# Kernel optimization log

Hardware: AMD Instinct MI355X
Metric: run time of the kernel (lower is better)

## Reference

```python
import jax, jax.numpy as jnp
import numpy as np

N = 50000      # nodes
E = 800000     # edges
D_IN = 128     # in_channels == hidden_channels
D_H = 128
R = 4          # num_relations
L = 3          # n_layers
D_MID = D_H // 4
D_OUT = 40
BN_EPS = 1e-5


def setup_inputs() -> dict:
    key = jax.random.key(0)
    ks = jax.random.split(key, 12)
    return {
        "x": jax.random.normal(ks[0], (N, D_IN), dtype=jnp.float32),
        "edge_index": jax.random.randint(ks[1], (2, E), 0, N, dtype=jnp.int64),
        "edge_type": jax.random.randint(ks[2], (E,), 0, R, dtype=jnp.int64),
        "W_skip": jax.random.normal(ks[3], (L, D_IN, D_H), dtype=jnp.float32) * 0.1,
        "W_film_skip": jax.random.normal(ks[4], (L, D_IN, 2 * D_H), dtype=jnp.float32) * 0.1,
        "W_rel": jax.random.normal(ks[5], (L, R, D_IN, D_H), dtype=jnp.float32) * 0.1,
        "W_film": jax.random.normal(ks[6], (L, R, D_IN, 2 * D_H), dtype=jnp.float32) * 0.1,
        "bn_w": jnp.ones((L, D_H), dtype=jnp.float32),
        "bn_b": jnp.zeros((L, D_H), dtype=jnp.float32),
        "lin1_w": jax.random.normal(ks[7], (D_H, D_MID), dtype=jnp.float32) * 0.1,
        "lin1_b": jnp.zeros((D_MID,), dtype=jnp.float32),
        "lin2_w": jax.random.normal(ks[8], (D_MID, D_OUT), dtype=jnp.float32) * 0.1,
        "lin2_b": jnp.zeros((D_OUT,), dtype=jnp.float32),
    }


def _film_conv(x, Wsk, Wfsk, Wr, Wf, src, dst, etype):
    # Self path: FiLM-modulated skip transform (PyG FiLMConv, act=ReLU).
    beta_s, gamma_s = jnp.split(x @ Wfsk, 2, axis=-1)  # split order: beta, gamma
    out = jax.nn.relu(gamma_s * (x @ Wsk) + beta_s)    # [N, D_H]
    # Per-relation node transforms (small GEMMs, avoids dynamic edge masking).
    xr = jnp.einsum('ni,rio->nro', x, Wr)              # [N, R, D_H]
    bg = jnp.einsum('ni,rio->nro', x, Wf)              # [N, R, 2*D_H]
    beta, gamma = jnp.split(bg, 2, axis=-1)            # each [N, R, D_H]
    # Messages: gamma_i * (W_r x_j) + beta_i, relation chosen per edge.
    msg = jax.nn.relu(gamma[dst, etype] * xr[src, etype] + beta[dst, etype])  # [E, D_H]
    # Mean aggregation per (target node, relation) subgraph, then sum relations.
    seg = dst * R + etype
    sums = jax.ops.segment_sum(msg, seg, num_segments=N * R)
    cnts = jax.ops.segment_sum(jnp.ones((msg.shape[0],), msg.dtype), seg, num_segments=N * R)
    mean = sums / jnp.maximum(cnts, 1.0)[:, None]      # [N*R, D_H]
    return out + mean.reshape(N, R, D_H).sum(axis=1)


def _batchnorm(h, w, b):
    mu = h.mean(axis=0)
    var = ((h - mu) ** 2).mean(axis=0)  # biased variance, as torch BN training
    return (h - mu) * jax.lax.rsqrt(var + BN_EPS) * w + b


def reference(x, edge_index, edge_type, W_skip, W_film_skip, W_rel, W_film,
              bn_w, bn_b, lin1_w, lin1_b, lin2_w, lin2_b):
    src, dst = edge_index[0], edge_index[1]
    h = x
    for l in range(L):
        h = _film_conv(h, W_skip[l], W_film_skip[l], W_rel[l], W_film[l], src, dst, edge_type)
        h = _batchnorm(h, bn_w[l], bn_b[l])
        # dropout treated as identity (deterministic reference)
    h = jax.nn.leaky_relu(h @ lin1_w + lin1_b, negative_slope=0.2)
    return h @ lin2_w + lin2_b
```

## Files before the change

### kernel.cpp

```cpp
#include <hip/hip_runtime.h>

#define N_NODES 50000
#define N_EDGES 800000
#define D 128
#define R_REL 4
#define L_LAYERS 3
#define M_SEG (N_NODES * R_REL)
#define NCOLS 384
#define BN_EPS 1e-5f

typedef unsigned short u16;
typedef __attribute__((ext_vector_type(8))) short short8v;
typedef __attribute__((ext_vector_type(4))) float f32x4;

static __device__ __forceinline__ u16 f2b(float f) {
    union { float f; unsigned int u; } a; a.f = f;
    unsigned int u = a.u;
    return (u16)((u + 0x7FFFu + ((u >> 16) & 1u)) >> 16);
}
static __device__ __forceinline__ float b2f(u16 b) {
    union { unsigned int u; float f; } a; a.u = ((unsigned int)b) << 16;
    return a.f;
}

__global__ void pack_w(const float* __restrict__ Wsk, const float* __restrict__ Wfsk,
                       const float* __restrict__ Wr, const float* __restrict__ Wf,
                       u16* __restrict__ Wpb) {
    int idx = blockIdx.x * 256 + threadIdx.x;
    if (idx >= L_LAYERS * 5 * NCOLS * D) return;
    int k = idx & 127;
    int rem = idx >> 7;
    int j = rem % NCOLS;
    int lp = rem / NCOLS;
    int l = lp / 5, p = lp % 5;
    float v;
    if (p == 0) {
        v = (j < D) ? Wsk[(l * D + k) * D + j] : Wfsk[(l * D + k) * 2 * D + (j - D)];
    } else {
        int r = p - 1;
        v = (j < D) ? Wr[((l * R_REL + r) * D + k) * D + j]
                    : Wf[((l * R_REL + r) * D + k) * 2 * D + (j - D)];
    }
    Wpb[idx] = f2b(v);
}

__global__ void cvt_bf16(const float* __restrict__ x, u16* __restrict__ xb) {
    int idx = blockIdx.x * 256 + threadIdx.x;
    if (idx >= N_NODES * D) return;
    xb[idx] = f2b(x[idx]);
}

__global__ void hist_k(const int* __restrict__ dst, const int* __restrict__ et,
                       int* __restrict__ cnt, int* __restrict__ rank) {
    int e = blockIdx.x * 256 + threadIdx.x;
    if (e >= N_EDGES) return;
    rank[e] = atomicAdd(&cnt[dst[e] * R_REL + et[e]], 1);
}

__global__ void scan_a(const int* __restrict__ cnt, int* __restrict__ bsum) {
    __shared__ int sm[256];
    int t = threadIdx.x;
    int idx = blockIdx.x * 256 + t;
    sm[t] = (idx < M_SEG) ? cnt[idx] : 0;
    __syncthreads();
    for (int s = 128; s > 0; s >>= 1) {
        if (t < s) sm[t] += sm[t + s];
        __syncthreads();
    }
    if (t == 0) bsum[blockIdx.x] = sm[0];
}

#define NB_SCAN 782
__global__ void scan_b(const int* __restrict__ bsum, int* __restrict__ bsumex, int* __restrict__ offs) {
    __shared__ int sm[1024];
    int t = threadIdx.x;
    int v = (t < NB_SCAN) ? bsum[t] : 0;
    sm[t] = v;
    __syncthreads();
    for (int d = 1; d < 1024; d <<= 1) {
        int add = (t >= d) ? sm[t - d] : 0;
        __syncthreads();
        sm[t] += add;
        __syncthreads();
    }
    if (t < NB_SCAN) bsumex[t] = sm[t] - v;
    if (t == NB_SCAN - 1) offs[M_SEG] = sm[t];
}

__global__ void scan_c(const int* __restrict__ cnt, const int* __restrict__ bsumex, int* __restrict__ offs) {
    __shared__ int sm[256];
    int t = threadIdx.x;
    int idx = blockIdx.x * 256 + t;
    int v = (idx < M_SEG) ? cnt[idx] : 0;
    sm[t] = v;
    __syncthreads();
    for (int d = 1; d < 256; d <<= 1) {
        int add = (t >= d) ? sm[t - d] : 0;
        __syncthreads();
        sm[t] += add;
        __syncthreads();
    }
    if (idx < M_SEG) offs[idx] = bsumex[blockIdx.x] + sm[t] - v;
}

__global__ void scatter_k(const int* __restrict__ src, const int* __restrict__ dst,
                          const int* __restrict__ et, const int* __restrict__ offs,
                          const int* __restrict__ rank, int* __restrict__ esrc) {
    int e = blockIdx.x * 256 + threadIdx.x;
    if (e >= N_EDGES) return;
    int seg = dst[e] * R_REL + et[e];
    esrc[offs[seg] + rank[e]] = src[e];
}

__global__ __launch_bounds__(512) void gemm_planes(const uint4* __restrict__ Aq,
                                                   const uint4* __restrict__ Bq,
                                                   u16* __restrict__ bufR) {
    __shared__ uint4 As[128 * 16];
    __shared__ u16 Cs[128 * 128];
    int t = threadIdx.x;
    int m0 = blockIdx.x * 128;
    int p = blockIdx.y;
#pragma unroll
    for (int i = 0; i < 4; ++i) {
        int idx = i * 512 + t;
        int row = idx >> 4, kk = idx & 15;
        int gr = m0 + row;
        if (gr >= N_NODES) gr = N_NODES - 1;
        As[(row << 4) + (kk ^ (row & 7))] = Aq[gr * 16 + kk];
    }
    __syncthreads();
    int lane = t & 63, w = t >> 6;
    int wr = w >> 2, wc = w & 3;
    int lr = lane & 15, lh = lane >> 4;
    short8v a[4][4];
#pragma unroll
    for (int m = 0; m < 4; ++m) {
        int row = wr * 64 + m * 16 + lr;
#pragma unroll
        for (int ks = 0; ks < 4; ++ks)
            a[m][ks] = *reinterpret_cast<const short8v*>(&As[(row << 4) + ((ks * 4 + lh) ^ (row & 7))]);
    }
    const uint4* Bp = Bq + (size_t)(1 + p) * NCOLS * 16;
    u16* Cp = bufR + (size_t)p * N_NODES * NCOLS;
    f32x4 zero = {0.f, 0.f, 0.f, 0.f};
    int srow = t >> 4, sslot = t & 15;
#pragma unroll
    for (int chunk = 0; chunk < 3; ++chunk) {
        int n0 = chunk * 128;
        f32x4 acc[4][2];
#pragma unroll
        for (int m = 0; m < 4; ++m)
#pragma unroll
            for (int n = 0; n < 2; ++n) acc[m][n] = zero;
#pragma unroll
        for (int ks = 0; ks < 4; ++ks) {
            short8v b[2];
#pragma unroll
            for (int n = 0; n < 2; ++n) {
                int row = n0 + wc * 32 + n * 16 + lr;
                b[n] = *reinterpret_cast<const short8v*>(&Bp[row * 16 + ks * 4 + lh]);
            }
#pragma unroll
            for (int m = 0; m < 4; ++m)
#pragma unroll
                for (int n = 0; n < 2; ++n)
                    acc[m][n] = __builtin_amdgcn_mfma_f32_16x16x32_bf16(a[m][ks], b[n], acc[m][n], 0, 0, 0);
        }
        __syncthreads();
#pragma unroll
        for (int m = 0; m < 4; ++m)
#pragma unroll
            for (int reg = 0; reg < 4; ++reg) {
                int row = wr * 64 + m * 16 + lh * 4 + reg;
#pragma unroll
                for (int n = 0; n < 2; ++n) {
                    int col = wc * 32 + n * 16 + lr;
                    Cs[row * 128 + (col ^ ((lh & 1) << 4))] = f2b(acc[m][n][reg]);
                }
            }
        __syncthreads();
#pragma unroll
        for (int it = 0; it < 4; ++it) {
            int row = it * 32 + srow;
            int gr = m0 + row;
            if (gr < N_NODES) {
                uint4 v = *reinterpret_cast<const uint4*>(
                    &Cs[row * 128 + ((sslot * 8) ^ (((row >> 2) & 1) << 4))]);
                *reinterpret_cast<uint4*>(&Cp[(size_t)gr * NCOLS + n0 + sslot * 8]) = v;
            }
        }
    }
}

__global__ __launch_bounds__(512) void gemm_self(const uint4* __restrict__ Aq,
                                                 const uint4* __restrict__ Bq,
                                                 u16* __restrict__ selfb) {
    __shared__ uint4 As[128 * 16];
    __shared__ u16 Cs[128 * 128];
    int t = threadIdx.x;
    int m0 = blockIdx.x * 128;
#pragma unroll
    for (int i = 0; i < 4; ++i) {
        int idx = i * 512 + t;
        int row = idx >> 4, kk = idx & 15;
        int gr = m0 + row;
        if (gr >= N_NODES) gr = N_NODES - 1;
        As[(row << 4) + (kk ^ (row & 7))] = Aq[gr * 16 + kk];
    }
    __syncthreads();
    int lane = t & 63, w = t >> 6;
    int wr = w >> 2, wc = w & 3;
    int lr = lane & 15, lh = lane >> 4;
    short8v a[4][4];
#pragma unroll
    for (int m = 0; m < 4; ++m) {
        int row = wr * 64 + m * 16 + lr;
#pragma unroll
        for (int ks = 0; ks < 4; ++ks)
            a[m][ks] = *reinterpret_cast<const short8v*>(&As[(row << 4) + ((ks * 4 + lh) ^ (row & 7))]);
    }
    f32x4 zero = {0.f, 0.f, 0.f, 0.f};
    f32x4 hx[4][2], hb[4][2];
#pragma unroll
    for (int chunk = 0; chunk < 3; ++chunk) {
        int n0 = chunk * 128;
        f32x4 acc[4][2];
#pragma unroll
        for (int m = 0; m < 4; ++m)
#pragma unroll
            for (int n = 0; n < 2; ++n) acc[m][n] = zero;
#pragma unroll
        for (int ks = 0; ks < 4; ++ks) {
            short8v b[2];
#pragma unroll
            for (int n = 0; n < 2; ++n) {
                int row = n0 + wc * 32 + n * 16 + lr;
                b[n] = *reinterpret_cast<const short8v*>(&Bq[row * 16 + ks * 4 + lh]);
            }
#pragma unroll
            for (int m = 0; m < 4; ++m)
#pragma unroll
                for (int n = 0; n < 2; ++n)
                    acc[m][n] = __builtin_amdgcn_mfma_f32_16x16x32_bf16(a[m][ks], b[n], acc[m][n], 0, 0, 0);
        }
        if (chunk == 0) {
#pragma unroll
            for (int m = 0; m < 4; ++m)
#pragma unroll
                for (int n = 0; n < 2; ++n) hx[m][n] = acc[m][n];
        } else if (chunk == 1) {
#pragma unroll
            for (int m = 0; m < 4; ++m)
#pragma unroll
                for (int n = 0; n < 2; ++n) hb[m][n] = acc[m][n];
        } else {
#pragma unroll
            for (int m = 0; m < 4; ++m)
#pragma unroll
                for (int reg = 0; reg < 4; ++reg) {
                    int row = wr * 64 + m * 16 + lh * 4 + reg;
#pragma unroll
                    for (int n = 0; n < 2; ++n) {
                        int col = wc * 32 + n * 16 + lr;
                        float h = fmaxf(acc[m][n][reg] * hx[m][n][reg] + hb[m][n][reg], 0.f);
                        Cs[row * 128 + (col ^ ((lh & 1) << 4))] = f2b(h);
                    }
                }
        }
    }
    __syncthreads();
    int srow = t >> 4, sslot = t & 15;
#pragma unroll
    for (int it = 0; it < 4; ++it) {
        int row = it * 32 + srow;
        int gr = m0 + row;
        if (gr < N_NODES) {
            uint4 v = *reinterpret_cast<const uint4*>(
                &Cs[row * 128 + ((sslot * 8) ^ (((row >> 2) & 1) << 4))]);
            *reinterpret_cast<uint4*>(&selfb[(size_t)gr * D + sslot * 8]) = v;
        }
    }
}

__global__ __launch_bounds__(256) void film_agg2(const u16* __restrict__ selfb, const u16* __restrict__ bufR,
                                                 const int* __restrict__ offs, const int* __restrict__ esrc,
                                                 float* __restrict__ acc) {
    int t = threadIdx.x;
    int n = blockIdx.x * 4 + (t >> 6);
    int lane = t & 63;
    int cg = (lane & 31) * 4;
    int half = lane >> 5;
    ushort4 hs = *reinterpret_cast<const ushort4*>(&selfb[(size_t)n * D + cg]);
    float h0 = b2f(hs.x), h1 = b2f(hs.y), h2 = b2f(hs.z), h3 = b2f(hs.w);
#pragma unroll
    for (int r = 0; r < R_REL; ++r) {
        const u16* B = bufR + (size_t)r * N_NODES * NCOLS;
        int seg = n * R_REL + r;
        int beg = offs[seg], end = offs[seg + 1];
        if (beg < end) {
            const u16* grow = B + (size_t)n * NCOLS;
            ushort4 b4 = *reinterpret_cast<const ushort4*>(&grow[128 + cg]);
            ushort4 g4 = *reinterpret_cast<const ushort4*>(&grow[256 + cg]);
            float g0 = b2f(g4.x), g1 = b2f(g4.y), g2 = b2f(g4.z), g3 = b2f(g4.w);
            float be0 = b2f(b4.x), be1 = b2f(b4.y), be2 = b2f(b4.z), be3 = b2f(b4.w);
            float s0 = 0.f, s1 = 0.f, s2 = 0.f, s3 = 0.f;
            for (int i = beg + half; i < end; i += 2) {
                int src = esrc[i];
                ushort4 x4 = *reinterpret_cast<const ushort4*>(&B[(size_t)src * NCOLS + cg]);
                s0 += fmaxf(g0 * b2f(x4.x) + be0, 0.f);
                s1 += fmaxf(g1 * b2f(x4.y) + be1, 0.f);
                s2 += fmaxf(g2 * b2f(x4.z) + be2, 0.f);
                s3 += fmaxf(g3 * b2f(x4.w) + be3, 0.f);
            }
            s0 += __shfl_xor(s0, 32);
            s1 += __shfl_xor(s1, 32);
            s2 += __shfl_xor(s2, 32);
            s3 += __shfl_xor(s3, 32);
            float inv = 1.f / (float)(end - beg);
            h0 += s0 * inv; h1 += s1 * inv; h2 += s2 * inv; h3 += s3 * inv;
        }
    }
    if (half == 0) {
        float4 o = make_float4(h0, h1, h2, h3);
        *reinterpret_cast<float4*>(&acc[(size_t)n * D + cg]) = o;
    }
}

__global__ __launch_bounds__(256) void bn_stats2(const float* __restrict__ acc, float* __restrict__ sums) {
    __shared__ float sm[256], sm2[256];
    int t = threadIdx.x;
    int c = t & 127, half = t >> 7;
    int rows = (N_NODES + gridDim.x - 1) / gridDim.x;
    int nb = blockIdx.x * rows;
    int n1 = min(nb + rows, N_NODES);
    float s = 0.f, s2 = 0.f;
    for (int n = nb + half; n < n1; n += 2) {
        float v = acc[n * D + c];
        s += v;
        s2 += v * v;
    }
    sm[t] = s; sm2[t] = s2;
    __syncthreads();
    if (t < 128) {
        atomicAdd(&sums[c], sm[t] + sm[t + 128]);
        atomicAdd(&sums[128 + c], sm2[t] + sm2[t + 128]);
    }
}

__global__ void bn_apply(const float* __restrict__ acc, const float* __restrict__ sums,
                         const float* __restrict__ w, const float* __restrict__ b,
                         u16* __restrict__ hb16) {
    int idx = blockIdx.x * 256 + threadIdx.x;
    if (idx >= N_NODES * D) return;
    int c = idx & 127;
    const float invn = 1.f / (float)N_NODES;
    float mu = sums[c] * invn;
    float var = sums[128 + c] * invn - mu * mu;
    float rs = rsqrtf(var + BN_EPS);
    hb16[idx] = f2b((acc[idx] - mu) * rs * w[c] + b[c]);
}

__global__ __launch_bounds__(128) void head_k(const u16* __restrict__ h, const float* __restrict__ w1,
                                              const float* __restrict__ b1, const float* __restrict__ w2,
                                              const float* __restrict__ b2, float* __restrict__ out) {
    __shared__ float hrow[128];
    __shared__ float part[128];
    __shared__ float mid[32];
    int n = blockIdx.x, t = threadIdx.x;
    hrow[t] = b2f(h[n * D + t]);
    __syncthreads();
    int m = t & 31, q = t >> 5;
    float p = 0.f;
#pragma unroll 8
    for (int k = q * 32; k < q * 32 + 32; ++k) p += hrow[k] * w1[k * 32 + m];
    part[t] = p;
    __syncthreads();
    if (t < 32) {
        float v = part[t] + part[t + 32] + part[t + 64] + part[t + 96] + b1[t];
        mid[t] = v > 0.f ? v : 0.2f * v;
    }
    __syncthreads();
    if (t < 40) {
        float o = b2[t];
#pragma unroll 8
        for (int mm = 0; mm < 32; ++mm) o += mid[mm] * w2[mm * 40 + t];
        out[n * 40 + t] = o;
    }
}

extern "C" void kernel_launch(void* const* d_in, const int* in_sizes, int n_in,
                              void* d_out, int out_size, void* d_ws, size_t ws_size,
                              hipStream_t stream) {
    const float* x    = (const float*)d_in[0];
    const int*   ei   = (const int*)d_in[1];
    const int*   et   = (const int*)d_in[2];
    const float* Wsk  = (const float*)d_in[3];
    const float* Wfsk = (const float*)d_in[4];
    const float* Wr   = (const float*)d_in[5];
    const float* Wf   = (const float*)d_in[6];
    const float* bnw  = (const float*)d_in[7];
    const float* bnb  = (const float*)d_in[8];
    const float* w1   = (const float*)d_in[9];
    const float* b1   = (const float*)d_in[10];
    const float* w2   = (const float*)d_in[11];
    const float* b2   = (const float*)d_in[12];
    const int* src = ei;
    const int* dst = ei + N_EDGES;

    char* ws = (char*)d_ws;
    size_t off = 0;
    auto alloc = [&](size_t bytes) -> void* {
        void* p = ws + off;
        off += (bytes + 255) & ~(size_t)255;
        return p;
    };
    u16*   Wpb  = (u16*)alloc((size_t)L_LAYERS * 5 * NCOLS * D * 2);
    u16*   inb  = (u16*)alloc((size_t)N_NODES * D * 2);
    float* acc  = (float*)alloc((size_t)N_NODES * D * 4);
    int*   cnt    = (int*)alloc((size_t)M_SEG * 4);
    float* bns    = (float*)alloc((size_t)L_LAYERS * 256 * 4);
    int*   offs   = (int*)alloc((size_t)(M_SEG + 1) * 4);
    int*   esrc   = (int*)alloc((size_t)N_EDGES * 4);
    int*   rank   = (int*)alloc((size_t)N_EDGES * 4);
    int*   bsum   = (int*)alloc(1024 * 4);
    int*   bsumex = (int*)alloc(1024 * 4);
    u16*   bufR   = (u16*)alloc((size_t)4 * N_NODES * NCOLS * 2);
    u16*   selfb  = (u16*)alloc((size_t)N_NODES * D * 2);

    hipMemsetAsync(cnt, 0, (size_t)M_SEG * 4 + (size_t)L_LAYERS * 1024, stream);

    pack_w<<<(L_LAYERS * 5 * NCOLS * D + 255) / 256, 256, 0, stream>>>(Wsk, Wfsk, Wr, Wf, Wpb);
    cvt_bf16<<<(N_NODES * D + 255) / 256, 256, 0, stream>>>(x, inb);
    hist_k<<<(N_EDGES + 255) / 256, 256, 0, stream>>>(dst, et, cnt, rank);
    scan_a<<<NB_SCAN, 256, 0, stream>>>(cnt, bsum);
    scan_b<<<1, 1024, 0, stream>>>(bsum, bsumex, offs);
    scan_c<<<NB_SCAN, 256, 0, stream>>>(cnt, bsumex, offs);
    scatter_k<<<(N_EDGES + 255) / 256, 256, 0, stream>>>(src, dst, et, offs, rank, esrc);

    const int nbm = (N_NODES + 127) / 128;
    for (int l = 0; l < L_LAYERS; ++l) {
        const uint4* Aq = (const uint4*)inb;
        const uint4* Wl = (const uint4*)(Wpb + (size_t)(l * 5) * NCOLS * D);
        gemm_planes<<<dim3(nbm, 4), 512, 0, stream>>>(Aq, Wl, bufR);
        gemm_self<<<dim3(nbm, 1), 512, 0, stream>>>(Aq, Wl, selfb);
        film_agg2<<<N_NODES / 4, 256, 0, stream>>>(selfb, bufR, offs, esrc, acc);
        bn_stats2<<<256, 256, 0, stream>>>(acc, bns + l * 256);
        bn_apply<<<(N_NODES * D + 255) / 256, 256, 0, stream>>>(acc, bns + l * 256, bnw + l * D, bnb + l * D, inb);
    }
    head_k<<<N_NODES, 128, 0, stream>>>(inb, w1, b1, w2, b2, (float*)d_out);
}
```

Baseline: 799.0 us.

## Merge relation and self GEMMs; split gather planes and process relations per quarter-wave

Merges the per-relation GEMM and the self-path GEMM into one launch with a fifth grid plane that applies the FiLM skip epilogue. The relation outputs are split into a compact x_r plane per relation ([R,N,128]) and a per-node beta/gamma block ([N,4*256]). Packing x_r this way makes the random per-edge gathers hit a denser 256-byte row rather than a 768-byte stride. The aggregation kernel now gives each relation to a 16-lane group with 8-wide bf16 loads, so all four relations run in parallel and are summed via shuffles. This removes a launch and the serial relation loop, but it can cause lane imbalance when segment lengths differ between relations.

```diff
diff --git a/kernel.cpp b/kernel.cpp
--- a/kernel.cpp
+++ b/kernel.cpp
@@ -112,9 +112,10 @@
     esrc[offs[seg] + rank[e]] = src[e];
 }
 
-__global__ __launch_bounds__(512) void gemm_planes(const uint4* __restrict__ Aq,
-                                                   const uint4* __restrict__ Bq,
-                                                   u16* __restrict__ bufR) {
+__global__ __launch_bounds__(512) void gemm_all(const uint4* __restrict__ Aq,
+                                                const uint4* __restrict__ Bq,
+                                                u16* __restrict__ xrp, u16* __restrict__ gbp,
+                                                u16* __restrict__ selfb) {
     __shared__ uint4 As[128 * 16];
     __shared__ u16 Cs[128 * 128];
     int t = threadIdx.x;
@@ -140,9 +141,9 @@
         for (int ks = 0; ks < 4; ++ks)
             a[m][ks] = *reinterpret_cast<const short8v*>(&As[(row << 4) + ((ks * 4 + lh) ^ (row & 7))]);
     }
-    const uint4* Bp = Bq + (size_t)(1 + p) * NCOLS * 16;
-    u16* Cp = bufR + (size_t)p * N_NODES * NCOLS;
+    const uint4* Bp = Bq + (size_t)((p < 4) ? (1 + p) : 0) * NCOLS * 16;
     f32x4 zero = {0.f, 0.f, 0.f, 0.f};
+    f32x4 hx[4][2], hb[4][2];
     int srow = t >> 4, sslot = t & 15;
 #pragma unroll
     for (int chunk = 0; chunk < 3; ++chunk) {
@@ -166,18 +167,63 @@
                 for (int n = 0; n < 2; ++n)
                     acc[m][n] = __builtin_amdgcn_mfma_f32_16x16x32_bf16(a[m][ks], b[n], acc[m][n], 0, 0, 0);
         }
-        __syncthreads();
-#pragma unroll
-        for (int m = 0; m < 4; ++m)
-#pragma unroll
-            for (int reg = 0; reg < 4; ++reg) {
-                int row = wr * 64 + m * 16 + lh * 4 + reg;
-#pragma unroll
-                for (int n = 0; n < 2; ++n) {
-                    int col = wc * 32 + n * 16 + lr;
-                    Cs[row * 128 + (col ^ ((lh & 1) << 4))] = f2b(acc[m][n][reg]);
+        if (p < 4) {
+            __syncthreads();
+#pragma unroll
+            for (int m = 0; m < 4; ++m)
+#pragma unroll
+                for (int reg = 0; reg < 4; ++reg) {
+                    int row = wr * 64 + m * 16 + lh * 4 + reg;
+#pragma unroll
+                    for (int n = 0; n < 2; ++n) {
+                        int col = wc * 32 + n * 16 + lr;
+                        Cs[row * 128 + (col ^ ((lh & 1) << 4))] = f2b(acc[m][n][reg]);
+                    }
+                }
+            __syncthreads();
+#pragma unroll
+            for (int it = 0; it < 4; ++it) {
+                int row = it * 32 + srow;
+                int gr = m0 + row;
+                if (gr < N_NODES) {
+                    uint4 v = *reinterpret_cast<const uint4*>(
+                        &Cs[row * 128 + ((sslot * 8) ^ (((row >> 2) & 1) << 4))]);
+                    if (chunk == 0)
+                        *reinterpret_cast<uint4*>(&xrp[((size_t)p * N_NODES + gr) * 128 + sslot * 8]) = v;
+                    else if (chunk == 1)
+                        *reinterpret_cast<uint4*>(&gbp[(size_t)gr * 1024 + p * 256 + sslot * 8]) = v;
+                    else
+                        *reinterpret_cast<uint4*>(&gbp[(size_t)gr * 1024 + p * 256 + 128 + sslot * 8]) = v;
                 }
             }
+        } else {
+            if (chunk == 0) {
+#pragma unroll
+                for (int m = 0; m < 4; ++m)
+#pragma unroll
+                    for (int n = 0; n < 2; ++n) hx[m][n] = acc[m][n];
+            } else if (chunk == 1) {
+#pragma unroll
+                for (int m = 0; m < 4; ++m)
+#pragma unroll
+                    for (int n = 0; n < 2; ++n) hb[m][n] = acc[m][n];
+            } else {
+#pragma unroll
+                for (int m = 0; m < 4; ++m)
+#pragma unroll
+                    for (int reg = 0; reg < 4; ++reg) {
+                        int row = wr * 64 + m * 16 + lh * 4 + reg;
+#pragma unroll
+                        for (int n = 0; n < 2; ++n) {
+                            int col = wc * 32 + n * 16 + lr;
+                            float h = fmaxf(acc[m][n][reg] * hx[m][n][reg] + hb[m][n][reg], 0.f);
+                            Cs[row * 128 + (col ^ ((lh & 1) << 4))] = f2b(h);
+                        }
+                    }
+            }
+        }
+    }
+    if (p == 4) {
         __syncthreads();
 #pragma unroll
         for (int it = 0; it < 4; ++it) {
@@ -186,143 +232,63 @@
             if (gr < N_NODES) {
                 uint4 v = *reinterpret_cast<const uint4*>(
                     &Cs[row * 128 + ((sslot * 8) ^ (((row >> 2) & 1) << 4))]);
-                *reinterpret_cast<uint4*>(&Cp[(size_t)gr * NCOLS + n0 + sslot * 8]) = v;
+                *reinterpret_cast<uint4*>(&selfb[(size_t)gr * D + sslot * 8]) = v;
             }
         }
     }
 }
 
-__global__ __launch_bounds__(512) void gemm_self(const uint4* __restrict__ Aq,
-                                                 const uint4* __restrict__ Bq,
-                                                 u16* __restrict__ selfb) {
-    __shared__ uint4 As[128 * 16];
-    __shared__ u16 Cs[128 * 128];
-    int t = threadIdx.x;
-    int m0 = blockIdx.x * 128;
-#pragma unroll
-    for (int i = 0; i < 4; ++i) {
-        int idx = i * 512 + t;
-        int row = idx >> 4, kk = idx & 15;
-        int gr = m0 + row;
-        if (gr >= N_NODES) gr = N_NODES - 1;
-        As[(row << 4) + (kk ^ (row & 7))] = Aq[gr * 16 + kk];
-    }
-    __syncthreads();
-    int lane = t & 63, w = t >> 6;
-    int wr = w >> 2, wc = w & 3;
-    int lr = lane & 15, lh = lane >> 4;
-    short8v a[4][4];
-#pragma unroll
-    for (int m = 0; m < 4; ++m) {
-        int row = wr * 64 + m * 16 + lr;
-#pragma unroll
-        for (int ks = 0; ks < 4; ++ks)
-            a[m][ks] = *reinterpret_cast<const short8v*>(&As[(row << 4) + ((ks * 4 + lh) ^ (row & 7))]);
-    }
-    f32x4 zero = {0.f, 0.f, 0.f, 0.f};
-    f32x4 hx[4][2], hb[4][2];
-#pragma unroll
-    for (int chunk = 0; chunk < 3; ++chunk) {
-        int n0 = chunk * 128;
-        f32x4 acc[4][2];
-#pragma unroll
-        for (int m = 0; m < 4; ++m)
-#pragma unroll
-            for (int n = 0; n < 2; ++n) acc[m][n] = zero;
-#pragma unroll
-        for (int ks = 0; ks < 4; ++ks) {
-            short8v b[2];
-#pragma unroll
-            for (int n = 0; n < 2; ++n) {
-                int row = n0 + wc * 32 + n * 16 + lr;
-                b[n] = *reinterpret_cast<const short8v*>(&Bq[row * 16 + ks * 4 + lh]);
-            }
-#pragma unroll
-            for (int m = 0; m < 4; ++m)
-#pragma unroll
-                for (int n = 0; n < 2; ++n)
-                    acc[m][n] = __builtin_amdgcn_mfma_f32_16x16x32_bf16(a[m][ks], b[n], acc[m][n], 0, 0, 0);
-        }
-        if (chunk == 0) {
-#pragma unroll
-            for (int m = 0; m < 4; ++m)
-#pragma unroll
-                for (int n = 0; n < 2; ++n) hx[m][n] = acc[m][n];
-        } else if (chunk == 1) {
-#pragma unroll
-            for (int m = 0; m < 4; ++m)
-#pragma unroll
-                for (int n = 0; n < 2; ++n) hb[m][n] = acc[m][n];
-        } else {
-#pragma unroll
-            for (int m = 0; m < 4; ++m)
-#pragma unroll
-                for (int reg = 0; reg < 4; ++reg) {
-                    int row = wr * 64 + m * 16 + lh * 4 + reg;
-#pragma unroll
-                    for (int n = 0; n < 2; ++n) {
-                        int col = wc * 32 + n * 16 + lr;
-                        float h = fmaxf(acc[m][n][reg] * hx[m][n][reg] + hb[m][n][reg], 0.f);
-                        Cs[row * 128 + (col ^ ((lh & 1) << 4))] = f2b(h);
-                    }
-                }
-        }
-    }
-    __syncthreads();
-    int srow = t >> 4, sslot = t & 15;
-#pragma unroll
-    for (int it = 0; it < 4; ++it) {
-        int row = it * 32 + srow;
-        int gr = m0 + row;
-        if (gr < N_NODES) {
-            uint4 v = *reinterpret_cast<const uint4*>(
-                &Cs[row * 128 + ((sslot * 8) ^ (((row >> 2) & 1) << 4))]);
-            *reinterpret_cast<uint4*>(&selfb[(size_t)gr * D + sslot * 8]) = v;
-        }
-    }
-}
-
-__global__ __launch_bounds__(256) void film_agg2(const u16* __restrict__ selfb, const u16* __restrict__ bufR,
+__global__ __launch_bounds__(256) void film_agg3(const u16* __restrict__ selfb, const u16* __restrict__ xrp,
+                                                 const u16* __restrict__ gbp,
                                                  const int* __restrict__ offs, const int* __restrict__ esrc,
                                                  float* __restrict__ acc) {
     int t = threadIdx.x;
     int n = blockIdx.x * 4 + (t >> 6);
     int lane = t & 63;
-    int cg = (lane & 31) * 4;
-    int half = lane >> 5;
-    ushort4 hs = *reinterpret_cast<const ushort4*>(&selfb[(size_t)n * D + cg]);
-    float h0 = b2f(hs.x), h1 = b2f(hs.y), h2 = b2f(hs.z), h3 = b2f(hs.w);
-#pragma unroll
-    for (int r = 0; r < R_REL; ++r) {
-        const u16* B = bufR + (size_t)r * N_NODES * NCOLS;
-        int seg = n * R_REL + r;
-        int beg = offs[seg], end = offs[seg + 1];
-        if (beg < end) {
-            const u16* grow = B + (size_t)n * NCOLS;
-            ushort4 b4 = *reinterpret_cast<const ushort4*>(&grow[128 + cg]);
-            ushort4 g4 = *reinterpret_cast<const ushort4*>(&grow[256 + cg]);
-            float g0 = b2f(g4.x), g1 = b2f(g4.y), g2 = b2f(g4.z), g3 = b2f(g4.w);
-            float be0 = b2f(b4.x), be1 = b2f(b4.y), be2 = b2f(b4.z), be3 = b2f(b4.w);
-            float s0 = 0.f, s1 = 0.f, s2 = 0.f, s3 = 0.f;
-            for (int i = beg + half; i < end; i += 2) {
-                int src = esrc[i];
-                ushort4 x4 = *reinterpret_cast<const ushort4*>(&B[(size_t)src * NCOLS + cg]);
-                s0 += fmaxf(g0 * b2f(x4.x) + be0, 0.f);
-                s1 += fmaxf(g1 * b2f(x4.y) + be1, 0.f);
-                s2 += fmaxf(g2 * b2f(x4.z) + be2, 0.f);
-                s3 += fmaxf(g3 * b2f(x4.w) + be3, 0.f);
-            }
-            s0 += __shfl_xor(s0, 32);
-            s1 += __shfl_xor(s1, 32);
-            s2 += __shfl_xor(s2, 32);
-            s3 += __shfl_xor(s3, 32);
-            float inv = 1.f / (float)(end - beg);
-            h0 += s0 * inv; h1 += s1 * inv; h2 += s2 * inv; h3 += s3 * inv;
+    int cq = lane & 15;
+    int rel = lane >> 4;
+    float h[8];
+#pragma unroll
+    for (int j = 0; j < 8; ++j) h[j] = 0.f;
+    int seg = n * R_REL + rel;
+    int beg = offs[seg], end = offs[seg + 1];
+    if (beg < end) {
+        uint4 bv = *reinterpret_cast<const uint4*>(&gbp[(size_t)n * 1024 + rel * 256 + cq * 8]);
+        uint4 gv = *reinterpret_cast<const uint4*>(&gbp[(size_t)n * 1024 + rel * 256 + 128 + cq * 8]);
+        const u16* bp = (const u16*)&bv;
+        const u16* gp = (const u16*)&gv;
+        float be[8], ga[8];
+#pragma unroll
+        for (int j = 0; j < 8; ++j) { be[j] = b2f(bp[j]); ga[j] = b2f(gp[j]); }
+        const u16* X = xrp + (size_t)rel * N_NODES * D;
+        float s[8];
+#pragma unroll
+        for (int j = 0; j < 8; ++j) s[j] = 0.f;
+        for (int i = beg; i < end; ++i) {
+            int src = esrc[i];
+            uint4 xv = *reinterpret_cast<const uint4*>(&X[(size_t)src * D + cq * 8]);
+            const u16* xp = (const u16*)&xv;
+#pragma unroll
+            for (int j = 0; j < 8; ++j) s[j] += fmaxf(ga[j] * b2f(xp[j]) + be[j], 0.f);
         }
-    }
-    if (half == 0) {
-        float4 o = make_float4(h0, h1, h2, h3);
-        *reinterpret_cast<float4*>(&acc[(size_t)n * D + cg]) = o;
+        float inv = 1.f / (float)(end - beg);
+#pragma unroll
+        for (int j = 0; j < 8; ++j) h[j] = s[j] * inv;
+    }
+#pragma unroll
+    for (int j = 0; j < 8; ++j) {
+        h[j] += __shfl_xor(h[j], 16);
+        h[j] += __shfl_xor(h[j], 32);
+    }
+    uint4 sv = *reinterpret_cast<const uint4*>(&selfb[(size_t)n * D + cq * 8]);
+    const u16* sp = (const u16*)&sv;
+#pragma unroll
+    for (int j = 0; j < 8; ++j) h[j] += b2f(sp[j]);
+    if (lane < 16) {
+        float4 o0 = make_float4(h[0], h[1], h[2], h[3]);
+        float4 o1 = make_float4(h[4], h[5], h[6], h[7]);
+        *reinterpret_cast<float4*>(&acc[(size_t)n * D + cq * 8]) = o0;
+        *reinterpret_cast<float4*>(&acc[(size_t)n * D + cq * 8 + 4]) = o1;
     }
 }
 
@@ -424,7 +390,8 @@
     int*   rank   = (int*)alloc((size_t)N_EDGES * 4);
     int*   bsum   = (int*)alloc(1024 * 4);
     int*   bsumex = (int*)alloc(1024 * 4);
-    u16*   bufR   = (u16*)alloc((size_t)4 * N_NODES * NCOLS * 2);
+    u16*   xrp    = (u16*)alloc((size_t)R_REL * N_NODES * D * 2);
+    u16*   gbp    = (u16*)alloc((size_t)N_NODES * R_REL * 256 * 2);
     u16*   selfb  = (u16*)alloc((size_t)N_NODES * D * 2);
 
     hipMemsetAsync(cnt, 0, (size_t)M_SEG * 4 + (size_t)L_LAYERS * 1024, stream);
@@ -439,11 +406,10 @@
 
     const int nbm = (N_NODES + 127) / 128;
     for (int l = 0; l < L_LAYERS; ++l) {
-        const uint4* Aq = (const uint4*)inb;
-        const uint4* Wl = (const uint4*)(Wpb + (size_t)(l * 5) * NCOLS * D);
-        gemm_planes<<<dim3(nbm, 4), 512, 0, stream>>>(Aq, Wl, bufR);
-        gemm_self<<<dim3(nbm, 1), 512, 0, stream>>>(Aq, Wl, selfb);
-        film_agg2<<<N_NODES / 4, 256, 0, stream>>>(selfb, bufR, offs, esrc, acc);
+        gemm_all<<<dim3(nbm, 5), 512, 0, stream>>>((const uint4*)inb,
+                                                   (const uint4*)(Wpb + (size_t)(l * 5) * NCOLS * D),
+                                                   xrp, gbp, selfb);
+        film_agg3<<<N_NODES / 4, 256, 0, stream>>>(selfb, xrp, gbp, offs, esrc, acc);
         bn_stats2<<<256, 256, 0, stream>>>(acc, bns + l * 256);
         bn_apply<<<(N_NODES * D + 255) / 256, 256, 0, stream>>>(acc, bns + l * 256, bnw + l * D, bnb + l * D, inb);
     }
```

Measured after the change: 761.3 us. 4.7% less time.
